# Performance work log

Measured on AMD Instinct MI355X. Metric: run time of the kernel, lower is better.

The kernel has to match this reference:

```python
import jax, jax.numpy as jnp
import numpy as np

NUM_HEADS = 64
D_K = 8  # n_wires of the quantum circuit


def setup_inputs() -> dict:
    key = jax.random.key(0)
    k1, k2, k3 = jax.random.split(key, 3)
    B, S, E = 8, 8192, NUM_HEADS * D_K
    x = jax.random.normal(k1, (B, S, E), dtype=jnp.float32)
    # trainable RX rotation angles, one per wire, shared across heads
    theta = jax.random.normal(k2, (D_K,), dtype=jnp.float32)
    # out_proj weight (torch nn.Linear stores [out_features, in_features]); bias=False
    W_out = jax.random.normal(k3, (E, E), dtype=jnp.float32) * 0.02
    return {"x": x, "theta": theta, "W_out": W_out}


def reference(x, theta, W_out):
    B, S, E = x.shape
    H, d = NUM_HEADS, D_K
    # Quantum circuit per (batch, seq, head) element:
    # RX(x_i) then RX(theta_i) on wire i from |0>, <Z_i> = cos(x_i + theta_i).
    xr = x.reshape(B, S, H, d)               # (B, S, H, d_k)
    A = jnp.cos(xr + theta)                  # broadcast theta over wires
    # torch stacks heads first -> (B, H, S, d), then .view(B, S, E) on the
    # contiguous buffer (a memory-layout reinterpretation, not a head-merge).
    A = jnp.transpose(A, (0, 2, 1, 3)).reshape(B, S, E)
    # out_proj: y = A @ W^T (no bias)
    return A @ W_out.T
```

## Files before the change

### kernel.cpp

```cpp
#include <hip/hip_runtime.h>
#include <hip/hip_bf16.h>

typedef __attribute__((ext_vector_type(8))) short short8;
typedef __attribute__((ext_vector_type(4))) float float4v;
typedef __attribute__((ext_vector_type(4))) unsigned int uint4v;
typedef __attribute__((ext_vector_type(2))) unsigned int uint2v;

#define SS 8192
#define EE 512
#define HH 64
#define NKB 16

__device__ __forceinline__ unsigned int f2bf1(float f) {
    unsigned int u = __builtin_bit_cast(unsigned int, f);
    return (u + 0x7fffu + ((u >> 16) & 1u)) >> 16;
}
__device__ __forceinline__ unsigned int pack2(float lo, float hi) {
    return f2bf1(lo) | (f2bf1(hi) << 16);
}
__device__ __forceinline__ void gl_lds16(const void* g, void* l) {
    __builtin_amdgcn_global_load_lds(
        (const __attribute__((address_space(1))) void*)g,
        (__attribute__((address_space(3))) void*)l, 16, 0, 0);
}

__global__ void w_prep(const float* __restrict__ W, unsigned short* __restrict__ Wws) {
    int idx = blockIdx.x * 256 + threadIdx.x;
    int r  = idx >> 7;
    int kg = idx & 127;
    int k  = kg * 4;
    float4v v = *(const float4v*)(W + (size_t)r * EE + k);
    int ntile = r >> 7, n = r & 127, kb = k >> 5, kk = k & 31;
    unsigned short* dst = Wws + (((size_t)(ntile * 16 + kb) * 128 + n) * 32 + kk);
    uint2v pk = { pack2(v.x, v.y), pack2(v.z, v.w) };
    *(uint2v*)dst = pk;
}

__global__ __launch_bounds__(256, 2)
void qmha_fused2(const float* __restrict__ x, const float* __restrict__ theta,
                 const unsigned short* __restrict__ Wws, float* __restrict__ out)
{
    __shared__ __attribute__((aligned(16))) unsigned short A_lds[HH * 512];
    __shared__ __attribute__((aligned(16))) unsigned short W_lds[2][128 * 32];

    const int bx    = blockIdx.x;
    const int ntile = (bx >> 3) & 3;
    const int p     = ((bx >> 5) << 3) | (bx & 7);
    const int b     = p >> 7;
    const int sc    = p & 127;

    const int t = threadIdx.x, lane = t & 63, wid = t >> 6;

    const unsigned short* Wtile = Wws + (size_t)ntile * 16 * 4096;

    const int woff = wid * 1024 + lane * 8;
    {
        gl_lds16(Wtile + woff,       (unsigned short*)W_lds[0] + woff);
        gl_lds16(Wtile + woff + 512, (unsigned short*)W_lds[0] + woff + 512);
    }

    const float th0 = theta[0], th1 = theta[1], th2 = theta[2], th3 = theta[3];
    const float th4 = theta[4], th5 = theta[5], th6 = theta[6], th7 = theta[7];

    {
        const float* xb = x + ((size_t)b * SS + (size_t)sc * 64) * EE + lane * 8;
        const int sw = lane & 7;
        #pragma unroll
        for (int it = 0; it < 16; ++it) {
            const int s_loc = wid * 16 + it;
            const float* px = xb + (size_t)s_loc * EE;
            float4v v0 = *(const float4v*)(px);
            float4v v1 = *(const float4v*)(px + 4);
            float c0 = __cosf(v0.x + th0);
            float c1 = __cosf(v0.y + th1);
            float c2 = __cosf(v0.z + th2);
            float c3 = __cosf(v0.w + th3);
            float c4 = __cosf(v1.x + th4);
            float c5 = __cosf(v1.y + th5);
            float c6 = __cosf(v1.z + th6);
            float c7 = __cosf(v1.w + th7);
            uint4v pk = { pack2(c0,c1), pack2(c2,c3), pack2(c4,c5), pack2(c6,c7) };
            *(uint4v*)&A_lds[lane * 512 + ((s_loc ^ sw) * 8)] = pk;
        }
    }

    float4v acc[2][4];
    #pragma unroll
    for (int i = 0; i < 2; ++i)
        #pragma unroll
        for (int j = 0; j < 4; ++j)
            acc[i][j] = (float4v){0.f, 0.f, 0.f, 0.f};

    const int m0  = (wid >> 1) * 32;
    const int n0l = (wid & 1) * 64;
    const int fr  = lane & 15;
    const int q   = lane >> 4;
    const int swA = fr & 7;
    const int aBase0 = (m0 + fr) * 512;
    const int aBase1 = aBase0 + 16 * 512;
    const int bOff   = (n0l + fr) * 32 + q * 8;

    __syncthreads();

    for (int kb = 0; kb < NKB; ++kb) {
        if (kb < NKB - 1) {
            const unsigned short* Ws = Wtile + (size_t)(kb + 1) * 4096;
            unsigned short* Wd = (unsigned short*)W_lds[(kb + 1) & 1];
            gl_lds16(Ws + woff,       Wd + woff);
            gl_lds16(Ws + woff + 512, Wd + woff + 512);
        }
        const unsigned short* Bbuf = (const unsigned short*)W_lds[kb & 1];
        const int g = ((kb * 4 + q) ^ swA) * 8;

        short8 a0 = *(const short8*)&A_lds[aBase0 + g];
        short8 a1 = *(const short8*)&A_lds[aBase1 + g];
        short8 b0 = *(const short8*)&Bbuf[bOff + 0 * 16 * 32];
        short8 b1 = *(const short8*)&Bbuf[bOff + 1 * 16 * 32];
        short8 b2 = *(const short8*)&Bbuf[bOff + 2 * 16 * 32];
        short8 b3 = *(const short8*)&Bbuf[bOff + 3 * 16 * 32];

        acc[0][0] = __builtin_amdgcn_mfma_f32_16x16x32_bf16(a0, b0, acc[0][0], 0, 0, 0);
        acc[0][1] = __builtin_amdgcn_mfma_f32_16x16x32_bf16(a0, b1, acc[0][1], 0, 0, 0);
        acc[0][2] = __builtin_amdgcn_mfma_f32_16x16x32_bf16(a0, b2, acc[0][2], 0, 0, 0);
        acc[0][3] = __builtin_amdgcn_mfma_f32_16x16x32_bf16(a0, b3, acc[0][3], 0, 0, 0);
        acc[1][0] = __builtin_amdgcn_mfma_f32_16x16x32_bf16(a1, b0, acc[1][0], 0, 0, 0);
        acc[1][1] = __builtin_amdgcn_mfma_f32_16x16x32_bf16(a1, b1, acc[1][1], 0, 0, 0);
        acc[1][2] = __builtin_amdgcn_mfma_f32_16x16x32_bf16(a1, b2, acc[1][2], 0, 0, 0);
        acc[1][3] = __builtin_amdgcn_mfma_f32_16x16x32_bf16(a1, b3, acc[1][3], 0, 0, 0);

        __syncthreads();
    }

    const int colbase = ntile * 128 + n0l + fr;
    #pragma unroll
    for (int mt = 0; mt < 2; ++mt) {
        #pragma unroll
        for (int r = 0; r < 4; ++r) {
            const int hrow = m0 + mt * 16 + q * 4 + r;
            float* po = out + ((size_t)b * SS + (size_t)hrow * 128 + sc) * EE + colbase;
            po[0 * 16] = acc[mt][0][r];
            po[1 * 16] = acc[mt][1][r];
            po[2 * 16] = acc[mt][2][r];
            po[3 * 16] = acc[mt][3][r];
        }
    }
}

#define AS 520
#define WSF 40
__global__ __launch_bounds__(256, 2)
void qmha_fused_fb(const float* __restrict__ x, const float* __restrict__ theta,
                   const float* __restrict__ W, float* __restrict__ out)
{
    __shared__ __attribute__((aligned(16))) unsigned short A_lds[HH * AS];
    __shared__ __attribute__((aligned(16))) unsigned short W_lds[128 * WSF];
    const int bx = blockIdx.x;
    const int ntile = (bx >> 3) & 3;
    const int p = ((bx >> 5) << 3) | (bx & 7);
    const int b = p >> 7;
    const int sc = p & 127;
    const int t = threadIdx.x, lane = t & 63, wid = t >> 6;
    const int wn = t >> 1, wk = (t & 1) * 16;
    const float* Wbase = W + (size_t)(ntile * 128 + wn) * EE + wk;
    float4v wv0 = *(const float4v*)(Wbase + 0);
    float4v wv1 = *(const float4v*)(Wbase + 4);
    float4v wv2 = *(const float4v*)(Wbase + 8);
    float4v wv3 = *(const float4v*)(Wbase + 12);
    const float th0 = theta[0], th1 = theta[1], th2 = theta[2], th3 = theta[3];
    const float th4 = theta[4], th5 = theta[5], th6 = theta[6], th7 = theta[7];
    {
        const float* xb = x + ((size_t)b * SS + (size_t)sc * 64) * EE + lane * 8;
        #pragma unroll
        for (int it = 0; it < 16; ++it) {
            const int s_loc = wid * 16 + it;
            const float* px = xb + (size_t)s_loc * EE;
            float4v v0 = *(const float4v*)(px);
            float4v v1 = *(const float4v*)(px + 4);
            float c0 = __cosf(v0.x + th0), c1 = __cosf(v0.y + th1);
            float c2 = __cosf(v0.z + th2), c3 = __cosf(v0.w + th3);
            float c4 = __cosf(v1.x + th4), c5 = __cosf(v1.y + th5);
            float c6 = __cosf(v1.z + th6), c7 = __cosf(v1.w + th7);
            uint4v pk = { pack2(c0,c1), pack2(c2,c3), pack2(c4,c5), pack2(c6,c7) };
            *(uint4v*)&A_lds[lane * AS + s_loc * 8] = pk;
        }
    }
    float4v acc[2][4];
    #pragma unroll
    for (int i = 0; i < 2; ++i)
        #pragma unroll
        for (int j = 0; j < 4; ++j)
            acc[i][j] = (float4v){0.f, 0.f, 0.f, 0.f};
    const int m0 = (wid >> 1) * 32, n0l = (wid & 1) * 64;
    const int fr = lane & 15, q = lane >> 4;
    const unsigned short* Arow0 = &A_lds[(m0 + fr) * AS + q * 8];
    const unsigned short* Arow1 = Arow0 + 16 * AS;
    const unsigned short* Wrow  = &W_lds[(n0l + fr) * WSF + q * 8];
    for (int kb = 0; kb < NKB; ++kb) {
        __syncthreads();
        {
            uint4v lo = { pack2(wv0.x, wv0.y), pack2(wv0.z, wv0.w),
                          pack2(wv1.x, wv1.y), pack2(wv1.z, wv1.w) };
            uint4v hi = { pack2(wv2.x, wv2.y), pack2(wv2.z, wv2.w),
                          pack2(wv3.x, wv3.y), pack2(wv3.z, wv3.w) };
            *(uint4v*)&W_lds[wn * WSF + wk]     = lo;
            *(uint4v*)&W_lds[wn * WSF + wk + 8] = hi;
        }
        if (kb < NKB - 1) {
            const float* Wn = Wbase + (size_t)(kb + 1) * 32;
            wv0 = *(const float4v*)(Wn + 0);
            wv1 = *(const float4v*)(Wn + 4);
            wv2 = *(const float4v*)(Wn + 8);
            wv3 = *(const float4v*)(Wn + 12);
        }
        __syncthreads();
        short8 a0 = *(const short8*)(Arow0 + kb * 32);
        short8 a1 = *(const short8*)(Arow1 + kb * 32);
        short8 b0 = *(const short8*)(Wrow + 0 * 16 * WSF);
        short8 b1 = *(const short8*)(Wrow + 1 * 16 * WSF);
        short8 b2 = *(const short8*)(Wrow + 2 * 16 * WSF);
        short8 b3 = *(const short8*)(Wrow + 3 * 16 * WSF);
        acc[0][0] = __builtin_amdgcn_mfma_f32_16x16x32_bf16(a0, b0, acc[0][0], 0, 0, 0);
        acc[0][1] = __builtin_amdgcn_mfma_f32_16x16x32_bf16(a0, b1, acc[0][1], 0, 0, 0);
        acc[0][2] = __builtin_amdgcn_mfma_f32_16x16x32_bf16(a0, b2, acc[0][2], 0, 0, 0);
        acc[0][3] = __builtin_amdgcn_mfma_f32_16x16x32_bf16(a0, b3, acc[0][3], 0, 0, 0);
        acc[1][0] = __builtin_amdgcn_mfma_f32_16x16x32_bf16(a1, b0, acc[1][0], 0, 0, 0);
        acc[1][1] = __builtin_amdgcn_mfma_f32_16x16x32_bf16(a1, b1, acc[1][1], 0, 0, 0);
        acc[1][2] = __builtin_amdgcn_mfma_f32_16x16x32_bf16(a1, b2, acc[1][2], 0, 0, 0);
        acc[1][3] = __builtin_amdgcn_mfma_f32_16x16x32_bf16(a1, b3, acc[1][3], 0, 0, 0);
    }
    const int colbase = ntile * 128 + n0l + fr;
    #pragma unroll
    for (int mt = 0; mt < 2; ++mt) {
        #pragma unroll
        for (int r = 0; r < 4; ++r) {
            const int hrow = m0 + mt * 16 + q * 4 + r;
            float* po = out + ((size_t)b * SS + (size_t)hrow * 128 + sc) * EE + colbase;
            po[0 * 16] = acc[mt][0][r];
            po[1 * 16] = acc[mt][1][r];
            po[2 * 16] = acc[mt][2][r];
            po[3 * 16] = acc[mt][3][r];
        }
    }
}

extern "C" void kernel_launch(void* const* d_in, const int* in_sizes, int n_in,
                              void* d_out, int out_size, void* d_ws, size_t ws_size,
                              hipStream_t stream) {
    const float* x     = (const float*)d_in[0];
    const float* theta = (const float*)d_in[1];
    const float* W     = (const float*)d_in[2];
    float* out         = (float*)d_out;

    if (ws_size >= (size_t)EE * EE * sizeof(unsigned short)) {
        unsigned short* Wws = (unsigned short*)d_ws;
        w_prep<<<dim3(256), dim3(256), 0, stream>>>(W, Wws);
        qmha_fused2<<<dim3(4096), dim3(256), 0, stream>>>(x, theta, Wws, out);
    } else {
        qmha_fused_fb<<<dim3(4096), dim3(256), 0, stream>>>(x, theta, W, out);
    }
}
```

Before: 284.1 us.

## Stage W tiles through registers with 4-deep prefetch and one barrier per step

Replaces the asynchronous global-to-LDS loads of the W tiles with ordinary global loads into registers, prefetched four k-blocks ahead. Each step stores its tile into the double-buffered LDS slot before a single barrier, so the trailing barrier is gone. The k-loop is fully unrolled, and MFMA issue priority is raised with s_setprio. The aim is to hide W fetch latency and cut synchronisation per step, at the cost of extra VGPRs for the staged tiles and explicit LDS store instructions.

```diff
diff --git a/kernel.cpp b/kernel.cpp
--- a/kernel.cpp
+++ b/kernel.cpp
@@ -37,7 +37,7 @@
 }
 
 __global__ __launch_bounds__(256, 2)
-void qmha_fused2(const float* __restrict__ x, const float* __restrict__ theta,
+void qmha_fused3(const float* __restrict__ x, const float* __restrict__ theta,
                  const unsigned short* __restrict__ Wws, float* __restrict__ out)
 {
     __shared__ __attribute__((aligned(16))) unsigned short A_lds[HH * 512];
@@ -52,11 +52,14 @@
     const int t = threadIdx.x, lane = t & 63, wid = t >> 6;
 
     const unsigned short* Wtile = Wws + (size_t)ntile * 16 * 4096;
-
     const int woff = wid * 1024 + lane * 8;
-    {
-        gl_lds16(Wtile + woff,       (unsigned short*)W_lds[0] + woff);
-        gl_lds16(Wtile + woff + 512, (unsigned short*)W_lds[0] + woff + 512);
+    const unsigned short* wsrc = Wtile + woff;
+
+    short8 wa[4], wb[4];
+    #pragma unroll
+    for (int s = 0; s < 4; ++s) {
+        wa[s] = *(const short8*)(wsrc + (size_t)s * 4096);
+        wb[s] = *(const short8*)(wsrc + (size_t)s * 4096 + 512);
     }
 
     const float th0 = theta[0], th1 = theta[1], th2 = theta[2], th3 = theta[3];
@@ -100,15 +103,22 @@
     const int aBase1 = aBase0 + 16 * 512;
     const int bOff   = (n0l + fr) * 32 + q * 8;
 
-    __syncthreads();
-
+    asm volatile("s_waitcnt lgkmcnt(0)" ::: "memory");
+    __builtin_amdgcn_s_barrier();
+
+    #pragma unroll
     for (int kb = 0; kb < NKB; ++kb) {
-        if (kb < NKB - 1) {
-            const unsigned short* Ws = Wtile + (size_t)(kb + 1) * 4096;
-            unsigned short* Wd = (unsigned short*)W_lds[(kb + 1) & 1];
-            gl_lds16(Ws + woff,       Wd + woff);
-            gl_lds16(Ws + woff + 512, Wd + woff + 512);
-        }
+        unsigned short* Wd = (unsigned short*)W_lds[kb & 1] + woff;
+        *(short8*)(Wd)       = wa[kb & 3];
+        *(short8*)(Wd + 512) = wb[kb & 3];
+        if (kb + 4 < NKB) {
+            wa[kb & 3] = *(const short8*)(wsrc + (size_t)(kb + 4) * 4096);
+            wb[kb & 3] = *(const short8*)(wsrc + (size_t)(kb + 4) * 4096 + 512);
+        }
+        asm volatile("s_waitcnt lgkmcnt(0)" ::: "memory");
+        __builtin_amdgcn_s_barrier();
+        asm volatile("" ::: "memory");
+
         const unsigned short* Bbuf = (const unsigned short*)W_lds[kb & 1];
         const int g = ((kb * 4 + q) ^ swA) * 8;
 
@@ -119,6 +129,7 @@
         short8 b2 = *(const short8*)&Bbuf[bOff + 2 * 16 * 32];
         short8 b3 = *(const short8*)&Bbuf[bOff + 3 * 16 * 32];
 
+        __builtin_amdgcn_s_setprio(1);
         acc[0][0] = __builtin_amdgcn_mfma_f32_16x16x32_bf16(a0, b0, acc[0][0], 0, 0, 0);
         acc[0][1] = __builtin_amdgcn_mfma_f32_16x16x32_bf16(a0, b1, acc[0][1], 0, 0, 0);
         acc[0][2] = __builtin_amdgcn_mfma_f32_16x16x32_bf16(a0, b2, acc[0][2], 0, 0, 0);
@@ -127,8 +138,7 @@
         acc[1][1] = __builtin_amdgcn_mfma_f32_16x16x32_bf16(a1, b1, acc[1][1], 0, 0, 0);
         acc[1][2] = __builtin_amdgcn_mfma_f32_16x16x32_bf16(a1, b2, acc[1][2], 0, 0, 0);
         acc[1][3] = __builtin_amdgcn_mfma_f32_16x16x32_bf16(a1, b3, acc[1][3], 0, 0, 0);
-
-        __syncthreads();
+        __builtin_amdgcn_s_setprio(0);
     }
 
     const int colbase = ntile * 128 + n0l + fr;
@@ -254,7 +264,7 @@
     if (ws_size >= (size_t)EE * EE * sizeof(unsigned short)) {
         unsigned short* Wws = (unsigned short*)d_ws;
         w_prep<<<dim3(256), dim3(256), 0, stream>>>(W, Wws);
-        qmha_fused2<<<dim3(4096), dim3(256), 0, stream>>>(x, theta, Wws, out);
+        qmha_fused3<<<dim3(4096), dim3(256), 0, stream>>>(x, theta, Wws, out);
     } else {
         qmha_fused_fb<<<dim3(4096), dim3(256), 0, stream>>>(x, theta, W, out);
     }
```

Result: faster. 274.3 us (-3.4%).

## Compute full output row tile per block with W streamed from global into registers

Applied to the files above, without the earlier changes.

Each block now computes all 512 output columns for its 64 rows, so the cosine of each x tile is computed once instead of four times across N-tiles, and the grid shrinks to 1024 blocks. W fragments are loaded directly from global/L2 into registers with a two-stage register double buffer, replacing the LDS double buffer and the per-step block barriers. W is re-laid out as k-block-major, the A tile uses row padding instead of an XOR swizzle, and s_setprio is raised around the MFMA bursts. The cost is 128 accumulator registers per thread plus 16 B-fragment registers, which risks spills or lower occupancy, and every block now rereads all of W from cache.

```diff
diff --git a/kernel.cpp b/kernel.cpp
--- a/kernel.cpp
+++ b/kernel.cpp
@@ -8,8 +8,8 @@
 
 #define SS 8192
 #define EE 512
-#define HH 64
 #define NKB 16
+#define AP 520
 
 __device__ __forceinline__ unsigned int f2bf1(float f) {
     unsigned int u = __builtin_bit_cast(unsigned int, f);
@@ -18,136 +18,128 @@
 __device__ __forceinline__ unsigned int pack2(float lo, float hi) {
     return f2bf1(lo) | (f2bf1(hi) << 16);
 }
-__device__ __forceinline__ void gl_lds16(const void* g, void* l) {
-    __builtin_amdgcn_global_load_lds(
-        (const __attribute__((address_space(1))) void*)g,
-        (__attribute__((address_space(3))) void*)l, 16, 0, 0);
-}
 
 __global__ void w_prep(const float* __restrict__ W, unsigned short* __restrict__ Wws) {
     int idx = blockIdx.x * 256 + threadIdx.x;
-    int r  = idx >> 7;
+    int n  = idx >> 7;
     int kg = idx & 127;
     int k  = kg * 4;
-    float4v v = *(const float4v*)(W + (size_t)r * EE + k);
-    int ntile = r >> 7, n = r & 127, kb = k >> 5, kk = k & 31;
-    unsigned short* dst = Wws + (((size_t)(ntile * 16 + kb) * 128 + n) * 32 + kk);
+    float4v v = *(const float4v*)(W + (size_t)n * EE + k);
+    int kb = k >> 5, kl = k & 31;
+    unsigned short* dst = Wws + ((size_t)kb * (EE * 32) + (size_t)n * 32 + kl);
     uint2v pk = { pack2(v.x, v.y), pack2(v.z, v.w) };
     *(uint2v*)dst = pk;
 }
 
 __global__ __launch_bounds__(256, 2)
-void qmha_fused2(const float* __restrict__ x, const float* __restrict__ theta,
+void qmha_fused5(const float* __restrict__ x, const float* __restrict__ theta,
                  const unsigned short* __restrict__ Wws, float* __restrict__ out)
 {
-    __shared__ __attribute__((aligned(16))) unsigned short A_lds[HH * 512];
-    __shared__ __attribute__((aligned(16))) unsigned short W_lds[2][128 * 32];
-
-    const int bx    = blockIdx.x;
-    const int ntile = (bx >> 3) & 3;
-    const int p     = ((bx >> 5) << 3) | (bx & 7);
-    const int b     = p >> 7;
-    const int sc    = p & 127;
-
+    __shared__ __attribute__((aligned(16))) unsigned short A_lds[64 * AP];
+
+    const int bx = blockIdx.x;
+    const int b  = bx >> 7;
+    const int sc = bx & 127;
     const int t = threadIdx.x, lane = t & 63, wid = t >> 6;
-
-    const unsigned short* Wtile = Wws + (size_t)ntile * 16 * 4096;
-
-    const int woff = wid * 1024 + lane * 8;
-    {
-        gl_lds16(Wtile + woff,       (unsigned short*)W_lds[0] + woff);
-        gl_lds16(Wtile + woff + 512, (unsigned short*)W_lds[0] + woff + 512);
-    }
+    const int fr = lane & 15, q = lane >> 4;
+
+    const unsigned short* wbase = Wws + ((size_t)(wid * 128 + fr) * 32 + q * 8);
+
+    short8 bA[8], bB[8];
+    #pragma unroll
+    for (int nt = 0; nt < 8; ++nt)
+        bA[nt] = *(const short8*)(wbase + nt * 512);
 
     const float th0 = theta[0], th1 = theta[1], th2 = theta[2], th3 = theta[3];
     const float th4 = theta[4], th5 = theta[5], th6 = theta[6], th7 = theta[7];
 
     {
-        const float* xb = x + ((size_t)b * SS + (size_t)sc * 64) * EE + lane * 8;
-        const int sw = lane & 7;
+        const float* xb = x + ((size_t)b * SS + (size_t)sc * 64 + (size_t)wid * 16) * EE + lane * 8;
+        unsigned short* aw = A_lds + lane * AP + wid * 128;
         #pragma unroll
         for (int it = 0; it < 16; ++it) {
-            const int s_loc = wid * 16 + it;
-            const float* px = xb + (size_t)s_loc * EE;
+            const float* px = xb + (size_t)it * EE;
             float4v v0 = *(const float4v*)(px);
             float4v v1 = *(const float4v*)(px + 4);
-            float c0 = __cosf(v0.x + th0);
-            float c1 = __cosf(v0.y + th1);
-            float c2 = __cosf(v0.z + th2);
-            float c3 = __cosf(v0.w + th3);
-            float c4 = __cosf(v1.x + th4);
-            float c5 = __cosf(v1.y + th5);
-            float c6 = __cosf(v1.z + th6);
-            float c7 = __cosf(v1.w + th7);
+            float c0 = __cosf(v0.x + th0), c1 = __cosf(v0.y + th1);
+            float c2 = __cosf(v0.z + th2), c3 = __cosf(v0.w + th3);
+            float c4 = __cosf(v1.x + th4), c5 = __cosf(v1.y + th5);
+            float c6 = __cosf(v1.z + th6), c7 = __cosf(v1.w + th7);
             uint4v pk = { pack2(c0,c1), pack2(c2,c3), pack2(c4,c5), pack2(c6,c7) };
-            *(uint4v*)&A_lds[lane * 512 + ((s_loc ^ sw) * 8)] = pk;
-        }
-    }
-
-    float4v acc[2][4];
-    #pragma unroll
-    for (int i = 0; i < 2; ++i)
-        #pragma unroll
-        for (int j = 0; j < 4; ++j)
+            *(uint4v*)(aw + it * 8) = pk;
+        }
+    }
+
+    __syncthreads();
+
+    float4v acc[4][8];
+    #pragma unroll
+    for (int i = 0; i < 4; ++i)
+        #pragma unroll
+        for (int j = 0; j < 8; ++j)
             acc[i][j] = (float4v){0.f, 0.f, 0.f, 0.f};
 
-    const int m0  = (wid >> 1) * 32;
-    const int n0l = (wid & 1) * 64;
-    const int fr  = lane & 15;
-    const int q   = lane >> 4;
-    const int swA = fr & 7;
-    const int aBase0 = (m0 + fr) * 512;
-    const int aBase1 = aBase0 + 16 * 512;
-    const int bOff   = (n0l + fr) * 32 + q * 8;
-
-    __syncthreads();
-
-    for (int kb = 0; kb < NKB; ++kb) {
-        if (kb < NKB - 1) {
-            const unsigned short* Ws = Wtile + (size_t)(kb + 1) * 4096;
-            unsigned short* Wd = (unsigned short*)W_lds[(kb + 1) & 1];
-            gl_lds16(Ws + woff,       Wd + woff);
-            gl_lds16(Ws + woff + 512, Wd + woff + 512);
-        }
-        const unsigned short* Bbuf = (const unsigned short*)W_lds[kb & 1];
-        const int g = ((kb * 4 + q) ^ swA) * 8;
-
-        short8 a0 = *(const short8*)&A_lds[aBase0 + g];
-        short8 a1 = *(const short8*)&A_lds[aBase1 + g];
-        short8 b0 = *(const short8*)&Bbuf[bOff + 0 * 16 * 32];
-        short8 b1 = *(const short8*)&Bbuf[bOff + 1 * 16 * 32];
-        short8 b2 = *(const short8*)&Bbuf[bOff + 2 * 16 * 32];
-        short8 b3 = *(const short8*)&Bbuf[bOff + 3 * 16 * 32];
-
-        acc[0][0] = __builtin_amdgcn_mfma_f32_16x16x32_bf16(a0, b0, acc[0][0], 0, 0, 0);
-        acc[0][1] = __builtin_amdgcn_mfma_f32_16x16x32_bf16(a0, b1, acc[0][1], 0, 0, 0);
-        acc[0][2] = __builtin_amdgcn_mfma_f32_16x16x32_bf16(a0, b2, acc[0][2], 0, 0, 0);
-        acc[0][3] = __builtin_amdgcn_mfma_f32_16x16x32_bf16(a0, b3, acc[0][3], 0, 0, 0);
-        acc[1][0] = __builtin_amdgcn_mfma_f32_16x16x32_bf16(a1, b0, acc[1][0], 0, 0, 0);
-        acc[1][1] = __builtin_amdgcn_mfma_f32_16x16x32_bf16(a1, b1, acc[1][1], 0, 0, 0);
-        acc[1][2] = __builtin_amdgcn_mfma_f32_16x16x32_bf16(a1, b2, acc[1][2], 0, 0, 0);
-        acc[1][3] = __builtin_amdgcn_mfma_f32_16x16x32_bf16(a1, b3, acc[1][3], 0, 0, 0);
-
-        __syncthreads();
-    }
-
-    const int colbase = ntile * 128 + n0l + fr;
-    #pragma unroll
-    for (int mt = 0; mt < 2; ++mt) {
+    const int aoff = fr * AP + q * 8;
+
+    #pragma unroll
+    for (int kb = 0; kb < NKB; kb += 2) {
+        {
+            const unsigned short* wn = wbase + (size_t)(kb + 1) * (EE * 32);
+            #pragma unroll
+            for (int nt = 0; nt < 8; ++nt)
+                bB[nt] = *(const short8*)(wn + nt * 512);
+        }
+        {
+            short8 af[4];
+            #pragma unroll
+            for (int mt = 0; mt < 4; ++mt)
+                af[mt] = *(const short8*)&A_lds[aoff + mt * 16 * AP + kb * 32];
+            __builtin_amdgcn_s_setprio(1);
+            #pragma unroll
+            for (int nt = 0; nt < 8; ++nt)
+                #pragma unroll
+                for (int mt = 0; mt < 4; ++mt)
+                    acc[mt][nt] = __builtin_amdgcn_mfma_f32_16x16x32_bf16(af[mt], bA[nt], acc[mt][nt], 0, 0, 0);
+            __builtin_amdgcn_s_setprio(0);
+        }
+        if (kb + 2 < NKB) {
+            const unsigned short* wn = wbase + (size_t)(kb + 2) * (EE * 32);
+            #pragma unroll
+            for (int nt = 0; nt < 8; ++nt)
+                bA[nt] = *(const short8*)(wn + nt * 512);
+        }
+        {
+            short8 af[4];
+            #pragma unroll
+            for (int mt = 0; mt < 4; ++mt)
+                af[mt] = *(const short8*)&A_lds[aoff + mt * 16 * AP + (kb + 1) * 32];
+            __builtin_amdgcn_s_setprio(1);
+            #pragma unroll
+            for (int nt = 0; nt < 8; ++nt)
+                #pragma unroll
+                for (int mt = 0; mt < 4; ++mt)
+                    acc[mt][nt] = __builtin_amdgcn_mfma_f32_16x16x32_bf16(af[mt], bB[nt], acc[mt][nt], 0, 0, 0);
+            __builtin_amdgcn_s_setprio(0);
+        }
+    }
+
+    float* outb = out + (size_t)b * (SS * EE) + (size_t)sc * EE + wid * 128 + fr;
+    #pragma unroll
+    for (int mt = 0; mt < 4; ++mt) {
         #pragma unroll
         for (int r = 0; r < 4; ++r) {
-            const int hrow = m0 + mt * 16 + q * 4 + r;
-            float* po = out + ((size_t)b * SS + (size_t)hrow * 128 + sc) * EE + colbase;
-            po[0 * 16] = acc[mt][0][r];
-            po[1 * 16] = acc[mt][1][r];
-            po[2 * 16] = acc[mt][2][r];
-            po[3 * 16] = acc[mt][3][r];
+            const int m = mt * 16 + q * 4 + r;
+            float* po = outb + (size_t)m * (128 * EE);
+            #pragma unroll
+            for (int nt = 0; nt < 8; ++nt)
+                po[nt * 16] = acc[mt][nt][r];
         }
     }
 }
 
 #define AS 520
 #define WSF 40
+#define HH 64
 __global__ __launch_bounds__(256, 2)
 void qmha_fused_fb(const float* __restrict__ x, const float* __restrict__ theta,
                    const float* __restrict__ W, float* __restrict__ out)
@@ -254,7 +246,7 @@
     if (ws_size >= (size_t)EE * EE * sizeof(unsigned short)) {
         unsigned short* Wws = (unsigned short*)d_ws;
         w_prep<<<dim3(256), dim3(256), 0, stream>>>(W, Wws);
-        qmha_fused2<<<dim3(4096), dim3(256), 0, stream>>>(x, theta, Wws, out);
+        qmha_fused5<<<dim3(1024), dim3(256), 0, stream>>>(x, theta, Wws, out);
     } else {
         qmha_fused_fb<<<dim3(4096), dim3(256), 0, stream>>>(x, theta, W, out);
     }
```

Result: faster. 257.7 us (-9.3%).
